# Optimization experiments

Hardware: AMD Instinct MI355X
Metric: run time of the kernel (lower is better)

The kernel has to match this reference:

```python
import jax, jax.numpy as jnp
import numpy as np

ALPHA = 0.2  # LeakyReLU negative slope


def setup_inputs() -> dict:
    key = jax.random.key(0)
    k1, k2, k3, k4 = jax.random.split(key, 4)
    B, N, in_dim, out_dim, n_heads = 4, 2048, 128, 32, 4
    H = jax.random.normal(k1, (B, N, in_dim), dtype=jnp.float32)
    adj = jax.random.randint(k2, (N, N), 0, 2).astype(jnp.float32)
    # xavier-uniform-like init for params
    limW = np.sqrt(6.0 / (in_dim + out_dim))
    W = jax.random.uniform(k3, (n_heads, in_dim, out_dim), minval=-limW, maxval=limW, dtype=jnp.float32)
    lima = np.sqrt(6.0 / (n_heads + 2 * out_dim))
    a = jax.random.uniform(k4, (n_heads, 2 * out_dim), minval=-lima, maxval=lima, dtype=jnp.float32)
    return {"H": H, "adj": adj, "W": W, "a": a}


def reference(H, adj, W, a):
    B, N, _ = H.shape
    n_heads, _, out_dim = W.shape
    # projected features: (B, H, N, F)
    Ht = jnp.einsum('bni,hio->bhno', H, W)
    # split attention vector: e_ij = leaky_relu(a_src . h_i + a_dst . h_j)
    a_src, a_dst = a[:, :out_dim], a[:, out_dim:]
    src = jnp.einsum('bhnf,hf->bhn', Ht, a_src)  # (B,H,N)
    dst = jnp.einsum('bhnf,hf->bhn', Ht, a_dst)  # (B,H,N)
    e = src[:, :, :, None] + dst[:, :, None, :]  # (B,H,N,N)
    e = jnp.where(e >= 0, e, ALPHA * e)          # leaky_relu
    mask = (adj + jnp.eye(N, dtype=adj.dtype)) != 0  # (N,N) bool, self-loops added
    e = jnp.where(mask[None, None], e, -jnp.inf)
    alpha = jax.nn.softmax(e, axis=-1)           # (B,H,N,N)
    H_new = jnp.einsum('bhnj,bhjf->bhnf', alpha, Ht)
    H_new = jnp.where(H_new > 0, H_new, jnp.expm1(H_new))  # ELU
    # concat heads: (B, N, n_heads*out_dim)
    H_new = jnp.transpose(H_new, (0, 2, 1, 3)).reshape(B, N, n_heads * out_dim)
    return H_new, alpha
```

## Files before the change

kernel.cpp:

```cpp
#include <hip/hip_runtime.h>
#include <hip/hip_bf16.h>
#include <math.h>


typedef float f32x4 __attribute__((ext_vector_type(4)));
typedef short bf16x8 __attribute__((ext_vector_type(8)));
typedef unsigned int u32;

#define LRELU 0.2f
#define LOG2E 1.44269504088896f
#define EXP2(x) __builtin_amdgcn_exp2f(x)

__device__ inline ushort f2b(float x) {
    unsigned int u = __float_as_uint(x);
    u += 0x7fffu + ((u >> 16) & 1u);
    return (ushort)(u >> 16);
}

__global__ __launch_bounds__(256) void k01(const float* __restrict__ adj,
                                           unsigned char* __restrict__ adjI,
                                           const float* __restrict__ H,
                                           const float* __restrict__ W,
                                           const float* __restrict__ a,
                                           __hip_bfloat16* __restrict__ HtT,
                                           float* __restrict__ src,
                                           float* __restrict__ dst) {
    __shared__ __align__(16) ushort Wbf[32 * 128];

    int bid = blockIdx.x;
    int t = threadIdx.x;

    if (bid >= 512) {
        int idx = (bid - 512) * 256 + t;
        int e0 = idx * 4;
        int row = e0 >> 11;
        int c0 = e0 & 2047;
        float4 v = *(const float4*)(adj + (size_t)e0);
        uchar4 o;
        o.x = (v.x != 0.f || c0     == row) ? 1 : 0;
        o.y = (v.y != 0.f || c0 + 1 == row) ? 1 : 0;
        o.z = (v.z != 0.f || c0 + 2 == row) ? 1 : 0;
        o.w = (v.w != 0.f || c0 + 3 == row) ? 1 : 0;
        *(uchar4*)(adjI + (size_t)e0) = o;
        return;
    }

    int ntile = bid & 31;
    int bh = bid >> 5;
    int b = bh >> 2, h = bh & 3;
    int lane = t & 63, w = t >> 6;
    int l15 = lane & 15, l4 = lane >> 4;

    #pragma unroll
    for (int u = 0; u < 16; ++u) {
        int idx = u * 256 + t;
        int i = idx >> 5, f = idx & 31;
        Wbf[(f * 128 + i) ^ ((f & 7) << 3)] = f2b(W[h * 4096 + idx]);
    }
    __syncthreads();

    int n = ntile * 64 + w * 16 + l15;
    const float* hrow = H + ((size_t)(b * 2048) + n) * 128;

    f32x4 acc0 = {0.f, 0.f, 0.f, 0.f};
    f32x4 acc1 = {0.f, 0.f, 0.f, 0.f};
    #pragma unroll
    for (int kc = 0; kc < 4; ++kc) {
        int k0 = kc * 32 + l4 * 8;
        float4 h0 = *(const float4*)(hrow + k0);
        float4 h1 = *(const float4*)(hrow + k0 + 4);
        union { u32 u[4]; bf16x8 v; } bu;
        asm("v_cvt_pk_bf16_f32 %0, %1, %2" : "=v"(bu.u[0]) : "v"(h0.x), "v"(h0.y));
        asm("v_cvt_pk_bf16_f32 %0, %1, %2" : "=v"(bu.u[1]) : "v"(h0.z), "v"(h0.w));
        asm("v_cvt_pk_bf16_f32 %0, %1, %2" : "=v"(bu.u[2]) : "v"(h1.x), "v"(h1.y));
        asm("v_cvt_pk_bf16_f32 %0, %1, %2" : "=v"(bu.u[3]) : "v"(h1.z), "v"(h1.w));
        bf16x8 bfrag = bu.v;
        bf16x8 af0 = *(const bf16x8*)&Wbf[(l15 * 128 + kc * 32 + l4 * 8) ^ ((l15 & 7) << 3)];
        bf16x8 af1 = *(const bf16x8*)&Wbf[((16 + l15) * 128 + kc * 32 + l4 * 8) ^ (((16 + l15) & 7) << 3)];
        acc0 = __builtin_amdgcn_mfma_f32_16x16x32_bf16(af0, bfrag, acc0, 0, 0, 0);
        acc1 = __builtin_amdgcn_mfma_f32_16x16x32_bf16(af1, bfrag, acc1, 0, 0, 0);
    }

    float sv = 0.f, dvv = 0.f;
    #pragma unroll
    for (int r = 0; r < 4; ++r) {
        int f0 = l4 * 4 + r;
        sv  += acc0[r] * a[h * 64 + f0]      + acc1[r] * a[h * 64 + 16 + f0];
        dvv += acc0[r] * a[h * 64 + 32 + f0] + acc1[r] * a[h * 64 + 48 + f0];
    }
    sv  += __shfl_xor(sv, 16);  sv  += __shfl_xor(sv, 32);
    dvv += __shfl_xor(dvv, 16); dvv += __shfl_xor(dvv, 32);
    if (l4 == 0) { src[bh * 2048 + n] = sv; dst[bh * 2048 + n] = dvv; }

    __syncthreads();
    ushort* T = Wbf;
    int nl = w * 16 + l15;
    #pragma unroll
    for (int r = 0; r < 4; ++r) {
        int f0 = l4 * 4 + r;
        T[f0 * 64 + nl]        = f2b(acc0[r]);
        T[(16 + f0) * 64 + nl] = f2b(acc1[r]);
    }
    __syncthreads();
    {
        int f = t >> 3, n8 = (t & 7) * 8;
        uint4 v = *(const uint4*)&T[f * 64 + n8];
        *(uint4*)((ushort*)HtT + (size_t)(bh * 32 + f) * 2048 + ntile * 64 + n8) = v;
    }
}

__global__ __launch_bounds__(256, 4) void k2_fused(const unsigned char* __restrict__ adjI,
                                                   const float* __restrict__ src,
                                                   const float* __restrict__ dst,
                                                   const __hip_bfloat16* __restrict__ HtT,
                                                   float* __restrict__ alpha,
                                                   float* __restrict__ outH) {
    __shared__ float dstS[2048];
    __shared__ float rowL[32], rowSrcS[32];
    __shared__ __align__(16) ushort As[2][32 * 128];

    int t = threadIdx.x;
    int mtile = blockIdx.x;
    int bh    = blockIdx.y;
    int lane = t & 63, w = t >> 6;
    int b = bh >> 2, h = bh & 3;
    int row0 = mtile * 32;

    const float4* dst4g = (const float4*)(dst + bh * 2048);
    #pragma unroll
    for (int u = 0; u < 2; ++u) {
        float4 v = dst4g[u * 256 + t];
        v.x *= LOG2E; v.y *= LOG2E; v.z *= LOG2E; v.w *= LOG2E;
        *(float4*)&dstS[(u * 256 + t) * 4] = v;
    }
    if (t < 32) rowSrcS[t] = src[bh * 2048 + row0 + t] * LOG2E;
    __syncthreads();

    for (int rr = 0; rr < 8; ++rr) {
        int r = w * 8 + rr;
        int gr = row0 + r;
        float sn = rowSrcS[r];
        const uint4* a16 = (const uint4*)(adjI + (size_t)gr * 2048);
        float S = 0.f;
        #pragma unroll
        for (int u = 0; u < 2; ++u) {
            uint4 ab = a16[u * 64 + lane];
            int jb = (u * 64 + lane) * 16;
            u32 words[4] = {ab.x, ab.y, ab.z, ab.w};
            #pragma unroll
            for (int wq = 0; wq < 4; ++wq) {
                float4 dv = *(const float4*)&dstS[jb + wq * 4];
                float dj[4] = {dv.x, dv.y, dv.z, dv.w};
                #pragma unroll
                for (int q = 0; q < 4; ++q) {
                    float ajf = (float)((words[wq] >> (8 * q)) & 0xffu);
                    float ee = sn + dj[q];
                    float vm = fmaxf(ee, LRELU * ee);
                    S = fmaf(EXP2(vm), ajf, S);
                }
            }
        }
        #pragma unroll
        for (int off = 32; off; off >>= 1) S += __shfl_xor(S, off);
        if (lane == 0) rowL[r] = -__log2f(S);
    }
    __syncthreads();

    f32x4 acc = {0.f, 0.f, 0.f, 0.f};
    int wr = w >> 1, wc = w & 1;
    int l15 = lane & 15, l4 = lane >> 4;
    int arow = wr * 16 + l15;
    const ushort* Bfp = (const ushort*)HtT + (size_t)(bh * 32 + wc * 16 + l15) * 2048 + l4 * 8;
    float* alphaRow = alpha + (size_t)(bh * 2048 + row0) * 2048;

    int sr = t >> 5;
    int sc4 = t & 31;

    float snR[4], LR[4];
    #pragma unroll
    for (int u = 0; u < 4; ++u) { snR[u] = rowSrcS[sr + u * 8]; LR[u] = rowL[sr + u * 8]; }

    auto loadA = [&](int k, u32* ar) {
        #pragma unroll
        for (int u = 0; u < 4; ++u)
            ar[u] = *(const u32*)(adjI + (size_t)(row0 + sr + u * 8) * 2048 + k * 128 + sc4 * 4);
    };
    auto loadB = [&](int k, bf16x8* br) {
        #pragma unroll
        for (int kk = 0; kk < 4; ++kk)
            br[kk] = *(const bf16x8*)(Bfp + (size_t)k * 128 + kk * 32);
    };
    auto stage = [&](int k, const u32* ar, ushort* Asb) {
        int jb = k * 128 + sc4 * 4;
        float4 dv = *(const float4*)&dstS[jb];
        float dj[4] = {dv.x, dv.y, dv.z, dv.w};
        #pragma unroll
        for (int u = 0; u < 4; ++u) {
            int r = sr + u * 8;
            float sn = snR[u], L = LR[u];
            u32 ab = ar[u];
            float o[4];
            #pragma unroll
            for (int q = 0; q < 4; ++q) {
                float ajf = (float)((ab >> (8 * q)) & 0xffu);
                float ee = sn + dj[q];
                float vm = fmaxf(ee + L, fmaf(ee, LRELU, L));
                o[q] = EXP2(vm) * ajf;
            }
            f32x4 ov = {o[0], o[1], o[2], o[3]};
            *(f32x4*)(alphaRow + (size_t)r * 2048 + jb) = ov;
            u32 lo, hi;
            asm("v_cvt_pk_bf16_f32 %0, %1, %2" : "=v"(lo) : "v"(o[0]), "v"(o[1]));
            asm("v_cvt_pk_bf16_f32 %0, %1, %2" : "=v"(hi) : "v"(o[2]), "v"(o[3]));
            uint2 pk = {lo, hi};
            *(uint2*)&Asb[(r * 128 + sc4 * 4) ^ ((r & 7) << 3)] = pk;
        }
    };
    auto mfmaPhase = [&](const bf16x8* br, const ushort* Asb) {
        #pragma unroll
        for (int kk = 0; kk < 4; ++kk) {
            bf16x8 af = *(const bf16x8*)&Asb[(arow * 128 + kk * 32 + l4 * 8) ^ ((arow & 7) << 3)];
            acc = __builtin_amdgcn_mfma_f32_16x16x32_bf16(af, br[kk], acc, 0, 0, 0);
        }
    };

    u32 aE[4], aO[4];
    bf16x8 bE[4], bO[4];
    loadA(0, aE); loadB(0, bE);

    for (int kp = 0; kp < 8; ++kp) {
        int ke = 2 * kp, ko = 2 * kp + 1;
        loadA(ko, aO); loadB(ko, bO);
        __builtin_amdgcn_sched_barrier(0);
        stage(ke, aE, As[0]);
        asm volatile("s_waitcnt lgkmcnt(0)" ::: "memory");
        __builtin_amdgcn_s_barrier();
        mfmaPhase(bE, As[0]);
        if (ko + 1 < 16) { loadA(ko + 1, aE); loadB(ko + 1, bE); }
        __builtin_amdgcn_sched_barrier(0);
        stage(ko, aO, As[1]);
        asm volatile("s_waitcnt lgkmcnt(0)" ::: "memory");
        __builtin_amdgcn_s_barrier();
        mfmaPhase(bO, As[1]);
    }

    #pragma unroll
    for (int q = 0; q < 4; ++q) {
        int node = row0 + wr * 16 + l4 * 4 + q;
        float v = acc[q];
        v = (v > 0.f) ? v : expm1f(v);
        outH[(size_t)(b * 2048 + node) * 128 + h * 32 + wc * 16 + l15] = v;
    }
}

extern "C" void kernel_launch(void* const* d_in, const int* in_sizes, int n_in,
                              void* d_out, int out_size, void* d_ws, size_t ws_size,
                              hipStream_t stream) {
    const float* H   = (const float*)d_in[0];
    const float* adj = (const float*)d_in[1];
    const float* W   = (const float*)d_in[2];
    const float* a   = (const float*)d_in[3];

    float* outH  = (float*)d_out;
    float* alpha = outH + (size_t)4 * 2048 * 128;

    char* ws = (char*)d_ws;
    __hip_bfloat16* HtT = (__hip_bfloat16*)ws;
    float* src = (float*)(ws + 2 * 1024 * 1024);
    float* dst = src + 32768;
    unsigned char* adjI = (unsigned char*)(ws + 2 * 1024 * 1024 + 256 * 1024);

    k01<<<4608, 256, 0, stream>>>(adj, adjI, H, W, a, HtT, src, dst);
    k2_fused<<<dim3(64, 16), 256, 0, stream>>>(adjI, src, dst, HtT, alpha, outH);
}
```

Baseline: 71.25 us.

## Process two row tiles per block, overlapping second tile's row-sum with first tile's main loop

```diff
diff --git a/kernel.cpp b/kernel.cpp
--- a/kernel.cpp
+++ b/kernel.cpp
@@ -117,14 +117,16 @@
                                                    float* __restrict__ outH) {
     __shared__ float dstS[2048];
     __shared__ float rowL[32], rowSrcS[32];
+    __shared__ float rowSrc1[32], rowS1[32];
     __shared__ __align__(16) ushort As[2][32 * 128];
 
     int t = threadIdx.x;
-    int mtile = blockIdx.x;
-    int bh    = blockIdx.y;
+    int pair = blockIdx.x;
+    int bh   = blockIdx.y;
     int lane = t & 63, w = t >> 6;
     int b = bh >> 2, h = bh & 3;
-    int row0 = mtile * 32;
+    int row0 = pair * 64;
+    int row1 = row0 + 32;
 
     const float4* dst4g = (const float4*)(dst + bh * 2048);
     #pragma unroll
@@ -133,7 +135,8 @@
         v.x *= LOG2E; v.y *= LOG2E; v.z *= LOG2E; v.w *= LOG2E;
         *(float4*)&dstS[(u * 256 + t) * 4] = v;
     }
-    if (t < 32) rowSrcS[t] = src[bh * 2048 + row0 + t] * LOG2E;
+    if (t < 32)      rowSrcS[t]      = src[bh * 2048 + row0 + t] * LOG2E;
+    else if (t < 64) rowSrc1[t - 32] = src[bh * 2048 + row1 + (t - 32)] * LOG2E;
     __syncthreads();
 
     for (int rr = 0; rr < 8; ++rr) {
@@ -166,29 +169,21 @@
     }
     __syncthreads();
 
-    f32x4 acc = {0.f, 0.f, 0.f, 0.f};
     int wr = w >> 1, wc = w & 1;
     int l15 = lane & 15, l4 = lane >> 4;
     int arow = wr * 16 + l15;
     const ushort* Bfp = (const ushort*)HtT + (size_t)(bh * 32 + wc * 16 + l15) * 2048 + l4 * 8;
-    float* alphaRow = alpha + (size_t)(bh * 2048 + row0) * 2048;
-
     int sr = t >> 5;
     int sc4 = t & 31;
 
     float snR[4], LR[4];
-    #pragma unroll
-    for (int u = 0; u < 4; ++u) { snR[u] = rowSrcS[sr + u * 8]; LR[u] = rowL[sr + u * 8]; }
+    float* aRowBase;
+    int rowBase;
 
     auto loadA = [&](int k, u32* ar) {
         #pragma unroll
         for (int u = 0; u < 4; ++u)
-            ar[u] = *(const u32*)(adjI + (size_t)(row0 + sr + u * 8) * 2048 + k * 128 + sc4 * 4);
-    };
-    auto loadB = [&](int k, bf16x8* br) {
-        #pragma unroll
-        for (int kk = 0; kk < 4; ++kk)
-            br[kk] = *(const bf16x8*)(Bfp + (size_t)k * 128 + kk * 32);
+            ar[u] = *(const u32*)(adjI + (size_t)(rowBase + sr + u * 8) * 2048 + k * 128 + sc4 * 4);
     };
     auto stage = [&](int k, const u32* ar, ushort* Asb) {
         int jb = k * 128 + sc4 * 4;
@@ -208,7 +203,7 @@
                 o[q] = EXP2(vm) * ajf;
             }
             f32x4 ov = {o[0], o[1], o[2], o[3]};
-            *(f32x4*)(alphaRow + (size_t)r * 2048 + jb) = ov;
+            *(f32x4*)(aRowBase + (size_t)r * 2048 + jb) = ov;
             u32 lo, hi;
             asm("v_cvt_pk_bf16_f32 %0, %1, %2" : "=v"(lo) : "v"(o[0]), "v"(o[1]));
             asm("v_cvt_pk_bf16_f32 %0, %1, %2" : "=v"(hi) : "v"(o[2]), "v"(o[3]));
@@ -216,6 +211,8 @@
             *(uint2*)&Asb[(r * 128 + sc4 * 4) ^ ((r & 7) << 3)] = pk;
         }
     };
+
+    f32x4 acc = {0.f, 0.f, 0.f, 0.f};
     auto mfmaPhase = [&](const bf16x8* br, const ushort* Asb) {
         #pragma unroll
         for (int kk = 0; kk < 4; ++kk) {
@@ -223,34 +220,97 @@
             acc = __builtin_amdgcn_mfma_f32_16x16x32_bf16(af, br[kk], acc, 0, 0, 0);
         }
     };
+    auto outEpi = [&](int rb) {
+        #pragma unroll
+        for (int q = 0; q < 4; ++q) {
+            int node = rb + wr * 16 + l4 * 4 + q;
+            float v = acc[q];
+            v = (v > 0.f) ? v : expm1f(v);
+            outH[(size_t)(b * 2048 + node) * 128 + h * 32 + wc * 16 + l15] = v;
+        }
+    };
+
+    int hi = lane >> 5;
+    int c32 = (lane & 31) * 4;
+    float snT1[4], Sacc[4] = {0.f, 0.f, 0.f, 0.f};
+    #pragma unroll
+    for (int rp = 0; rp < 4; ++rp) snT1[rp] = rowSrc1[w * 8 + rp * 2 + hi];
+
+    rowBase = row0;
+    aRowBase = alpha + (size_t)(bh * 2048 + row0) * 2048;
+    #pragma unroll
+    for (int u = 0; u < 4; ++u) { snR[u] = rowSrcS[sr + u * 8]; LR[u] = rowL[sr + u * 8]; }
 
     u32 aE[4], aO[4];
-    bf16x8 bE[4], bO[4];
-    loadA(0, aE); loadB(0, bE);
-
-    for (int kp = 0; kp < 8; ++kp) {
-        int ke = 2 * kp, ko = 2 * kp + 1;
-        loadA(ko, aO); loadB(ko, bO);
+    loadA(0, aE);
+    for (int kc = 0; kc < 16; ++kc) {
+        const u32* aC = (kc & 1) ? aO : aE;
+        u32*       aN = (kc & 1) ? aE : aO;
+        bf16x8 bf[4];
+        #pragma unroll
+        for (int kk = 0; kk < 4; ++kk)
+            bf[kk] = *(const bf16x8*)(Bfp + (size_t)kc * 128 + kk * 32);
+        u32 ab1[4];
+        #pragma unroll
+        for (int rp = 0; rp < 4; ++rp)
+            ab1[rp] = *(const u32*)(adjI + (size_t)(row1 + w * 8 + rp * 2 + hi) * 2048 + kc * 128 + c32);
+        if (kc < 15) loadA(kc + 1, aN);
         __builtin_amdgcn_sched_barrier(0);
-        stage(ke, aE, As[0]);
+        stage(kc, aC, As[kc & 1]);
+        {
+            float4 dv = *(const float4*)&dstS[kc * 128 + c32];
+            float dj[4] = {dv.x, dv.y, dv.z, dv.w};
+            #pragma unroll
+            for (int rp = 0; rp < 4; ++rp) {
+                float sn = snT1[rp];
+                u32 ab = ab1[rp];
+                #pragma unroll
+                for (int q = 0; q < 4; ++q) {
+                    float ajf = (float)((ab >> (8 * q)) & 0xffu);
+                    float ee = sn + dj[q];
+                    float vm = fmaxf(ee, LRELU * ee);
+                    Sacc[rp] = fmaf(EXP2(vm), ajf, Sacc[rp]);
+                }
+            }
+        }
         asm volatile("s_waitcnt lgkmcnt(0)" ::: "memory");
         __builtin_amdgcn_s_barrier();
-        mfmaPhase(bE, As[0]);
-        if (ko + 1 < 16) { loadA(ko + 1, aE); loadB(ko + 1, bE); }
+        mfmaPhase(bf, As[kc & 1]);
+    }
+    outEpi(row0);
+
+    #pragma unroll
+    for (int rp = 0; rp < 4; ++rp) {
+        float s = Sacc[rp];
+        s += __shfl_xor(s, 1);  s += __shfl_xor(s, 2);  s += __shfl_xor(s, 4);
+        s += __shfl_xor(s, 8);  s += __shfl_xor(s, 16);
+        if ((lane & 31) == 0) rowS1[w * 8 + rp * 2 + hi] = s;
+    }
+    asm volatile("s_waitcnt lgkmcnt(0)" ::: "memory");
+    __builtin_amdgcn_s_barrier();
+
+    rowBase = row1;
+    aRowBase = alpha + (size_t)(bh * 2048 + row1) * 2048;
+    #pragma unroll
+    for (int u = 0; u < 4; ++u) { snR[u] = rowSrc1[sr + u * 8]; LR[u] = -__log2f(rowS1[sr + u * 8]); }
+    acc[0] = acc[1] = acc[2] = acc[3] = 0.f;
+
+    loadA(0, aE);
+    for (int kc = 0; kc < 16; ++kc) {
+        const u32* aC = (kc & 1) ? aO : aE;
+        u32*       aN = (kc & 1) ? aE : aO;
+        bf16x8 bf[4];
+        #pragma unroll
+        for (int kk = 0; kk < 4; ++kk)
+            bf[kk] = *(const bf16x8*)(Bfp + (size_t)kc * 128 + kk * 32);
+        if (kc < 15) loadA(kc + 1, aN);
         __builtin_amdgcn_sched_barrier(0);
-        stage(ko, aO, As[1]);
+        stage(kc, aC, As[kc & 1]);
         asm volatile("s_waitcnt lgkmcnt(0)" ::: "memory");
         __builtin_amdgcn_s_barrier();
-        mfmaPhase(bO, As[1]);
-    }
-
-    #pragma unroll
-    for (int q = 0; q < 4; ++q) {
-        int node = row0 + wr * 16 + l4 * 4 + q;
-        float v = acc[q];
-        v = (v > 0.f) ? v : expm1f(v);
-        outH[(size_t)(b * 2048 + node) * 128 + h * 32 + wc * 16 + l15] = v;
-    }
+        mfmaPhase(bf, As[kc & 1]);
+    }
+    outEpi(row1);
 }
 
 extern "C" void kernel_launch(void* const* d_in, const int* in_sizes, int n_in,
@@ -271,5 +331,5 @@
     unsigned char* adjI = (unsigned char*)(ws + 2 * 1024 * 1024 + 256 * 1024);
 
     k01<<<4608, 256, 0, stream>>>(adj, adjI, H, W, a, HtT, src, dst);
-    k2_fused<<<dim3(64, 16), 256, 0, stream>>>(adjI, src, dst, HtT, alpha, outH);
+    k2_fused<<<dim3(32, 16), 256, 0, stream>>>(adjI, src, dst, HtT, alpha, outH);
 }
```

New measurement: 80.68 us. 1.13x slower.

## Move softmax row-sum computation into adjacency conversion kernel

Applied to the files above, without the earlier changes.

```diff
diff --git a/kernel.cpp b/kernel.cpp
--- a/kernel.cpp
+++ b/kernel.cpp
@@ -17,36 +17,17 @@
     return (ushort)(u >> 16);
 }
 
-__global__ __launch_bounds__(256) void k01(const float* __restrict__ adj,
-                                           unsigned char* __restrict__ adjI,
-                                           const float* __restrict__ H,
-                                           const float* __restrict__ W,
-                                           const float* __restrict__ a,
-                                           __hip_bfloat16* __restrict__ HtT,
-                                           float* __restrict__ src,
-                                           float* __restrict__ dst) {
+__global__ __launch_bounds__(256) void kA_ht(const float* __restrict__ H,
+                                             const float* __restrict__ W,
+                                             const float* __restrict__ a,
+                                             __hip_bfloat16* __restrict__ HtT,
+                                             float* __restrict__ src,
+                                             float* __restrict__ dst) {
     __shared__ __align__(16) ushort Wbf[32 * 128];
 
-    int bid = blockIdx.x;
     int t = threadIdx.x;
-
-    if (bid >= 512) {
-        int idx = (bid - 512) * 256 + t;
-        int e0 = idx * 4;
-        int row = e0 >> 11;
-        int c0 = e0 & 2047;
-        float4 v = *(const float4*)(adj + (size_t)e0);
-        uchar4 o;
-        o.x = (v.x != 0.f || c0     == row) ? 1 : 0;
-        o.y = (v.y != 0.f || c0 + 1 == row) ? 1 : 0;
-        o.z = (v.z != 0.f || c0 + 2 == row) ? 1 : 0;
-        o.w = (v.w != 0.f || c0 + 3 == row) ? 1 : 0;
-        *(uchar4*)(adjI + (size_t)e0) = o;
-        return;
-    }
-
-    int ntile = bid & 31;
-    int bh = bid >> 5;
+    int ntile = blockIdx.x;
+    int bh = blockIdx.y;
     int b = bh >> 2, h = bh & 3;
     int lane = t & 63, w = t >> 6;
     int l15 = lane & 15, l4 = lane >> 4;
@@ -109,9 +90,71 @@
     }
 }
 
+__global__ __launch_bounds__(256) void k0S(const float* __restrict__ adj,
+                                           const float* __restrict__ src,
+                                           const float* __restrict__ dst,
+                                           unsigned char* __restrict__ adjI,
+                                           float* __restrict__ rowLG) {
+    __shared__ __align__(16) unsigned char aS[2 * 2048];
+
+    int t = threadIdx.x;
+    int row0 = blockIdx.x * 2;
+    int lane = t & 63, w = t >> 6;
+
+    #pragma unroll
+    for (int u = 0; u < 4; ++u) {
+        int s = u * 256 + t;
+        int e0 = s * 4;
+        int r = e0 >> 11, c = e0 & 2047;
+        float4 v = *(const float4*)(adj + (size_t)(row0 + r) * 2048 + c);
+        uchar4 o;
+        o.x = (v.x != 0.f || c     == row0 + r) ? 1 : 0;
+        o.y = (v.y != 0.f || c + 1 == row0 + r) ? 1 : 0;
+        o.z = (v.z != 0.f || c + 2 == row0 + r) ? 1 : 0;
+        o.w = (v.w != 0.f || c + 3 == row0 + r) ? 1 : 0;
+        *(uchar4*)(adjI + (size_t)(row0 + r) * 2048 + c) = o;
+        *(uchar4*)&aS[r * 2048 + c] = o;
+    }
+    __syncthreads();
+
+    const u32* aSu = (const u32*)aS;
+    #pragma unroll
+    for (int i = 0; i < 4; ++i) {
+        int bh = w + i * 4;
+        float4 dv[8];
+        #pragma unroll
+        for (int j = 0; j < 8; ++j) {
+            float4 v = *(const float4*)(dst + (size_t)bh * 2048 + j * 256 + lane * 4);
+            v.x *= LOG2E; v.y *= LOG2E; v.z *= LOG2E; v.w *= LOG2E;
+            dv[j] = v;
+        }
+        #pragma unroll
+        for (int r = 0; r < 2; ++r) {
+            float sn = src[bh * 2048 + row0 + r] * LOG2E;
+            float S = 0.f;
+            #pragma unroll
+            for (int j = 0; j < 8; ++j) {
+                u32 ab = aSu[r * 512 + j * 64 + lane];
+                float dj[4] = {dv[j].x, dv[j].y, dv[j].z, dv[j].w};
+                #pragma unroll
+                for (int q = 0; q < 4; ++q) {
+                    float ajf = (float)((ab >> (8 * q)) & 0xffu);
+                    float ee = sn + dj[q];
+                    float vm = fmaxf(ee, LRELU * ee);
+                    S = fmaf(EXP2(vm), ajf, S);
+                }
+            }
+            #pragma unroll
+            for (int off = 32; off; off >>= 1) S += __shfl_xor(S, off);
+            if (lane == 0) rowLG[bh * 2048 + row0 + r] = -__log2f(S);
+        }
+    }
+}
+
 __global__ __launch_bounds__(256, 4) void k2_fused(const unsigned char* __restrict__ adjI,
                                                    const float* __restrict__ src,
                                                    const float* __restrict__ dst,
+                                                   const float* __restrict__ rowLG,
                                                    const __hip_bfloat16* __restrict__ HtT,
                                                    float* __restrict__ alpha,
                                                    float* __restrict__ outH) {
@@ -133,36 +176,9 @@
         v.x *= LOG2E; v.y *= LOG2E; v.z *= LOG2E; v.w *= LOG2E;
         *(float4*)&dstS[(u * 256 + t) * 4] = v;
     }
-    if (t < 32) rowSrcS[t] = src[bh * 2048 + row0 + t] * LOG2E;
-    __syncthreads();
-
-    for (int rr = 0; rr < 8; ++rr) {
-        int r = w * 8 + rr;
-        int gr = row0 + r;
-        float sn = rowSrcS[r];
-        const uint4* a16 = (const uint4*)(adjI + (size_t)gr * 2048);
-        float S = 0.f;
-        #pragma unroll
-        for (int u = 0; u < 2; ++u) {
-            uint4 ab = a16[u * 64 + lane];
-            int jb = (u * 64 + lane) * 16;
-            u32 words[4] = {ab.x, ab.y, ab.z, ab.w};
-            #pragma unroll
-            for (int wq = 0; wq < 4; ++wq) {
-                float4 dv = *(const float4*)&dstS[jb + wq * 4];
-                float dj[4] = {dv.x, dv.y, dv.z, dv.w};
-                #pragma unroll
-                for (int q = 0; q < 4; ++q) {
-                    float ajf = (float)((words[wq] >> (8 * q)) & 0xffu);
-                    float ee = sn + dj[q];
-                    float vm = fmaxf(ee, LRELU * ee);
-                    S = fmaf(EXP2(vm), ajf, S);
-                }
-            }
-        }
-        #pragma unroll
-        for (int off = 32; off; off >>= 1) S += __shfl_xor(S, off);
-        if (lane == 0) rowL[r] = -__log2f(S);
+    if (t < 32) {
+        rowSrcS[t] = src[bh * 2048 + row0 + t] * LOG2E;
+        rowL[t]    = rowLG[bh * 2048 + row0 + t];
     }
     __syncthreads();
 
@@ -266,10 +282,12 @@
 
     char* ws = (char*)d_ws;
     __hip_bfloat16* HtT = (__hip_bfloat16*)ws;
-    float* src = (float*)(ws + 2 * 1024 * 1024);
-    float* dst = src + 32768;
-    unsigned char* adjI = (unsigned char*)(ws + 2 * 1024 * 1024 + 256 * 1024);
-
-    k01<<<4608, 256, 0, stream>>>(adj, adjI, H, W, a, HtT, src, dst);
-    k2_fused<<<dim3(64, 16), 256, 0, stream>>>(adjI, src, dst, HtT, alpha, outH);
-}
+    float* src   = (float*)(ws + 2 * 1024 * 1024);
+    float* dst   = src + 32768;
+    float* rowLG = dst + 32768;
+    unsigned char* adjI = (unsigned char*)(ws + 2 * 1024 * 1024 + 512 * 1024);
+
+    kA_ht<<<dim3(32, 16), 256, 0, stream>>>(H, W, a, HtT, src, dst);
+    k0S<<<1024, 256, 0, stream>>>(adj, src, dst, adjI, rowLG);
+    k2_fused<<<dim3(64, 16), 256, 0, stream>>>(adjI, src, dst, rowLG, HtT, alpha, outH);
+}
```

Measured after the change: 84.29 us. 1.18x slower.
